# Performance work log

Hardware: AMD Instinct MI355X
Metric: run time of the kernel (lower is better)

The kernel has to match this reference:

```python
import jax, jax.numpy as jnp
import numpy as np
from jax import lax

N_GRAPHS = 256
N_NODES = 128      # nodes per graph (fixed-size batching)
N_TPLT = 16
N_TPLT_NODES = 10
N_FEAT = 128
AVG_DEG = 8
EPS = 0.1          # entropic regularization for the GW solver
OUTER_ITERS = 5    # outer mirror-descent (entropic GW) iterations
SINKHORN_ITERS = 20


def setup_inputs() -> dict:
    key = jax.random.key(0)
    k1, k2, k3, k4, k5 = jax.random.split(key, 5)
    x = jax.random.normal(k1, (N_GRAPHS * N_NODES, N_FEAT), jnp.float32)
    # per-graph random edges with global node ids (PyG convention)
    n_e = N_NODES * AVG_DEG
    src = jax.random.randint(k2, (N_GRAPHS, n_e), 0, N_NODES)
    dst = jax.random.randint(k3, (N_GRAPHS, n_e), 0, N_NODES)
    off = (jnp.arange(N_GRAPHS) * N_NODES)[:, None]
    edge_index = jnp.stack([(src + off).reshape(-1), (dst + off).reshape(-1)]).astype(jnp.int32)
    batch = jnp.repeat(jnp.arange(N_GRAPHS, dtype=jnp.int32), N_NODES)
    # template parameters (symmetric uniform adjacencies, normal features, zero q0 -> uniform weights)
    A0 = jax.random.uniform(k4, (N_TPLT, N_TPLT_NODES, N_TPLT_NODES), jnp.float32)
    tplt_adjacencies = 0.5 * (A0 + jnp.swapaxes(A0, 1, 2))
    tplt_features = jax.random.normal(k5, (N_TPLT, N_TPLT_NODES, N_FEAT), jnp.float32)
    q0 = jnp.zeros((N_TPLT, N_TPLT_NODES), jnp.float32)
    return {"x": x, "edge_index": edge_index, "batch": batch,
            "tplt_adjacencies": tplt_adjacencies, "tplt_features": tplt_features, "q0": q0}


def _gw_distances(C1, C2, p, q):
    # C1: [B,N,N] graph adjacencies, C2: [T,M,M] templates, p: [N], q: [T,M]
    # square-loss GW decomposition (Peyre et al.): f1=a^2, f2=b^2, h1=a, h2=2b
    B, N = C1.shape[0], C1.shape[1]
    T, M = C2.shape[0], C2.shape[1]
    f1p = jnp.einsum('bij,j->bi', C1 * C1, p)          # [B,N]
    f2q = jnp.einsum('tij,tj->ti', C2 * C2, q)         # [T,M]
    constC = f1p[:, None, :, None] + f2q[None, :, None, :]  # [B,T,N,M]

    def tens(P):
        # constC - h1(C1) P h2(C2)^T
        cross = jnp.einsum('bik,btkm,tjm->btij', C1, P, 2.0 * C2)
        return constC - cross

    P0 = jnp.broadcast_to(p[None, None, :, None] * q[None, :, None, :], (B, T, N, M))

    def outer(P, _):
        cost = 2.0 * tens(P)                     # GW gradient
        K = jnp.exp(-cost / EPS)                 # [B,T,N,M]
        u0 = jnp.ones((B, T, N), K.dtype)
        v0 = jnp.ones((B, T, M), K.dtype)

        def inner(carry, _):
            u, v = carry
            u = p[None, None, :] / jnp.einsum('btnm,btm->btn', K, v)
            v = q[None, :, :] / jnp.einsum('btnm,btn->btm', K, u)
            return (u, v), None

        (u, v), _ = lax.scan(inner, (u0, v0), None, length=SINKHORN_ITERS)
        P = u[..., :, None] * K * v[..., None, :]
        return P, None

    P, _ = lax.scan(outer, P0, None, length=OUTER_ITERS)
    return jnp.sum(tens(P) * P, axis=(2, 3))     # [B,T]


def reference(x, edge_index, batch, tplt_adjacencies, tplt_features, q0):
    # q = softmax(q0, dim=1): template node weights
    q = jax.nn.softmax(q0, axis=1)
    # dense per-graph adjacency from the sparse edge list
    g = batch[edge_index[0]]
    src = edge_index[0] - g * N_NODES
    dst = edge_index[1] - g * N_NODES
    C1 = jnp.zeros((N_GRAPHS, N_NODES, N_NODES), x.dtype)
    C1 = C1.at[g, src, dst].set(1.0)
    C1 = jnp.maximum(C1, jnp.swapaxes(C1, 1, 2))  # undirected
    p = jnp.full((N_NODES,), 1.0 / N_NODES, x.dtype)  # uniform graph node weights
    # fused=False: pure Gromov-Wasserstein, node features are not used
    return _gw_distances(C1, tplt_adjacencies, p, q)
```

## Files before the change

### kernel.cpp

```cpp
#include <hip/hip_runtime.h>

#define NGRAPH 256
#define NN     128
#define NT     16
#define NM     10
#define OUTER_IT 5
#define SINK_IT  20

#define SC1  28.85390081777927f
#define SC2  57.70780163555854f

typedef unsigned long long u64;
typedef float v2f __attribute__((ext_vector_type(2)));
typedef float v4f __attribute__((ext_vector_type(4)));

static __device__ __forceinline__ v2f pkfma(v2f a, v2f b, v2f c) {
  return __builtin_elementwise_fma(a, b, c);
}
static __device__ __forceinline__ v2f bc2(float s) { return (v2f){s, s}; }

template <int CTRL>
__device__ __forceinline__ float dpp_add(float a) {
  int t = __builtin_amdgcn_update_dpp(0, __float_as_int(a), CTRL, 0xf, 0xf, true);
  return a + __int_as_float(t);
}
__device__ __forceinline__ float allsum32(float x) {
  x = dpp_add<0xB1>(x);
  x = dpp_add<0x4E>(x);
  x = dpp_add<0x141>(x);
  x = dpp_add<0x140>(x);
  int sw = __builtin_amdgcn_ds_swizzle(__float_as_int(x), 0x401F);
  return x + __int_as_float(sw);
}

__global__ __launch_bounds__(64, 2)
void tgw_kernel(const int* __restrict__ ei,
                const float* __restrict__ tadj,
                const float* __restrict__ q0g,
                float* __restrict__ out,
                int E, int ne) {
  const int lane = threadIdx.x;
  const int p    = lane >> 5;
  const int sub  = lane & 31;
  const int b    = blockIdx.x >> 3;
  const int t0   = (blockIdx.x & 7) * 2;

  __shared__ __align__(16) unsigned adj[NN][4];
  __shared__ __align__(16) float Pls[2][NN][12];
  __shared__ __align__(16) v2f C2T[2][NM][6];
  __shared__ float q0s[2][NM];

  for (int i = lane; i < NN * 4; i += 64) (&adj[0][0])[i] = 0u;
  for (int i = lane; i < 2 * NM * 5; i += 64) {
    int tt = i / 50, r = i % 50, m = r / 5, jp = r % 5;
    const float* bp = tadj + (t0 + tt) * NM * NM + m;
    C2T[tt][m][jp] = (v2f){bp[(2 * jp) * NM], bp[(2 * jp + 1) * NM]} * SC2;
  }
  if (lane < 2 * NM) q0s[lane / NM][lane % NM] = q0g[t0 * NM + lane];
  __syncthreads();

  const int* srcp = ei;
  const int* dstp = ei + E;
  const int ebase = b * ne;
  for (int e = lane; e < ne; e += 64) {
    int s = srcp[ebase + e] & (NN - 1);
    int d = dstp[ebase + e] & (NN - 1);
    atomicOr(&adj[s][d >> 5], 1u << (d & 31));
    atomicOr(&adj[d][s >> 5], 1u << (s & 31));
  }
  __syncthreads();

  float qv[NM];
  {
    float mx = q0s[p][0];
    #pragma unroll
    for (int j = 1; j < NM; ++j) mx = fmaxf(mx, q0s[p][j]);
    float s = 0.f;
    #pragma unroll
    for (int j = 0; j < NM; ++j) { qv[j] = __expf(q0s[p][j] - mx); s += qv[j]; }
    float inv = __builtin_amdgcn_rcpf(s);
    #pragma unroll
    for (int j = 0; j < NM; ++j) qv[j] *= inv;
  }
  v2f q2[5];
  #pragma unroll
  for (int jp = 0; jp < 5; ++jp) q2[jp] = (v2f){qv[2 * jp], qv[2 * jp + 1]};

  v2f fq2[5], qC2T[5];
  {
    #pragma unroll
    for (int jp = 0; jp < 5; ++jp) { fq2[jp] = (v2f){0.f, 0.f}; qC2T[jp] = (v2f){0.f, 0.f}; }
    #pragma unroll
    for (int m = 0; m < NM; ++m) {
      v2f qb = bc2(qv[m]);
      #pragma unroll
      for (int jp = 0; jp < 5; ++jp) {
        v2f c = C2T[p][m][jp];
        fq2[jp]  = pkfma(c * c, qb, fq2[jp]);
        qC2T[jp] = pkfma(c, qb, qC2T[jp]);
      }
    }
    const float f = -1.0f / (4.0f * SC1);
    #pragma unroll
    for (int jp = 0; jp < 5; ++jp) fq2[jp] *= f;
  }

  const float pw = 1.0f / 128.0f;
  float f1p[4], m1f1[4];
  #pragma unroll
  for (int c = 0; c < 4; ++c) {
    uint4 mm = *(const uint4*)&adj[sub + 32 * c][0];
    u64 m0 = mm.x | ((u64)mm.y << 32), m1 = mm.z | ((u64)mm.w << 32);
    f1p[c]  = (float)(__popcll(m0) + __popcll(m1)) * pw;
    m1f1[c] = -SC1 * f1p[c];
  }

  const float* Pbase = &Pls[p][0][0];
  auto gatherRow = [&](int r, v2f* S2) {
    uint4 mm = *(const uint4*)&adj[r][0];
    u64 m0 = mm.x | ((u64)mm.y << 32), m1 = mm.z | ((u64)mm.w << 32);
    #pragma unroll
    for (int h = 0; h < 5; ++h) S2[h] = (v2f){0.f, 0.f};
    while (m0) {
      int k = (int)__builtin_ctzll(m0); m0 &= m0 - 1;
      const float* row = Pbase + k * 12;
      v4f A = *(const v4f*)row;
      v4f B = *(const v4f*)(row + 4);
      v2f C = *(const v2f*)(row + 8);
      S2[0] += A.xy; S2[1] += A.zw; S2[2] += B.xy; S2[3] += B.zw; S2[4] += C;
    }
    while (m1) {
      int k = 64 + (int)__builtin_ctzll(m1); m1 &= m1 - 1;
      const float* row = Pbase + k * 12;
      v4f A = *(const v4f*)row;
      v4f B = *(const v4f*)(row + 4);
      v2f C = *(const v2f*)(row + 8);
      S2[0] += A.xy; S2[1] += A.zw; S2[2] += B.xy; S2[3] += B.zw; S2[4] += C;
    }
  };

  auto costFromS = [&](float Sm[4][NM], v2f arg2[4][5]) {
    #pragma unroll
    for (int c = 0; c < 4; ++c) {
      v2f ib = fq2[0] + bc2(m1f1[c]);
      arg2[c][0] = ib;
      #pragma unroll
      for (int jp = 1; jp < 5; ++jp) arg2[c][jp] = fq2[jp] + bc2(m1f1[c]);
    }
    #pragma unroll
    for (int m = 0; m < NM; ++m) {
      v4f X = *(const v4f*)&C2T[p][m][0];
      v4f Y = *(const v4f*)&C2T[p][m][2];
      v2f Z = *(const v2f*)&C2T[p][m][4];
      #pragma unroll
      for (int c = 0; c < 4; ++c) {
        v2f sb = bc2(Sm[c][m]);
        arg2[c][0] = pkfma(sb, X.xy, arg2[c][0]);
        arg2[c][1] = pkfma(sb, X.zw, arg2[c][1]);
        arg2[c][2] = pkfma(sb, Y.xy, arg2[c][2]);
        arg2[c][3] = pkfma(sb, Y.zw, arg2[c][3]);
        arg2[c][4] = pkfma(sb, Z,    arg2[c][4]);
      }
    }
  };

  v2f K2[4][5], v2[5], arg2[4][5];
  float uu[4];

  for (int o = 0; o < OUTER_IT; ++o) {
    if (o == 0) {
      #pragma unroll
      for (int c = 0; c < 4; ++c) {
        v2f fb = bc2(f1p[c]);
        v2f ob = bc2(m1f1[c]);
        #pragma unroll
        for (int jp = 0; jp < 5; ++jp)
          arg2[c][jp] = pkfma(fb, qC2T[jp], fq2[jp] + ob);
      }
    } else {
      float Sm[4][NM];
      #pragma unroll
      for (int c = 0; c < 4; ++c) {
        v2f S2[5];
        gatherRow(sub + 32 * c, S2);
        #pragma unroll
        for (int h = 0; h < 5; ++h) { Sm[c][2 * h] = S2[h].x; Sm[c][2 * h + 1] = S2[h].y; }
      }
      costFromS(Sm, arg2);
    }
    #pragma unroll
    for (int c = 0; c < 4; ++c)
      #pragma unroll
      for (int jp = 0; jp < 5; ++jp)
        K2[c][jp] = (v2f){exp2f(arg2[c][jp].x), exp2f(arg2[c][jp].y)};

    #pragma unroll
    for (int jp = 0; jp < 5; ++jp) v2[jp] = (v2f){1.f, 1.f};
    for (int it = 0; it < SINK_IT; ++it) {
      #pragma unroll
      for (int c = 0; c < 4; ++c) {
        v2f d2 = K2[c][0] * v2[0];
        d2 = pkfma(K2[c][1], v2[1], d2);
        d2 = pkfma(K2[c][2], v2[2], d2);
        d2 = pkfma(K2[c][3], v2[3], d2);
        d2 = pkfma(K2[c][4], v2[4], d2);
        uu[c] = pw * __builtin_amdgcn_rcpf(d2.x + d2.y);
      }
      #pragma unroll
      for (int jp = 0; jp < 5; ++jp) {
        v2f w2 = K2[0][jp] * bc2(uu[0]);
        w2 = pkfma(K2[1][jp], bc2(uu[1]), w2);
        w2 = pkfma(K2[2][jp], bc2(uu[2]), w2);
        w2 = pkfma(K2[3][jp], bc2(uu[3]), w2);
        float cx = allsum32(w2.x);
        float cy = allsum32(w2.y);
        v2[jp] = (v2f){q2[jp].x * __builtin_amdgcn_rcpf(cx),
                       q2[jp].y * __builtin_amdgcn_rcpf(cy)};
      }
    }

    __syncthreads();
    #pragma unroll
    for (int c = 0; c < 4; ++c) {
      v2f ub = bc2(uu[c]);
      v2f x0 = K2[c][0] * ub * v2[0];
      v2f x1 = K2[c][1] * ub * v2[1];
      v2f x2 = K2[c][2] * ub * v2[2];
      v2f x3 = K2[c][3] * ub * v2[3];
      v2f x4 = K2[c][4] * ub * v2[4];
      float* row = &Pls[p][sub + 32 * c][0];
      *(v4f*)row       = (v4f){x0.x, x0.y, x1.x, x1.y};
      *(v4f*)(row + 4) = (v4f){x2.x, x2.y, x3.x, x3.y};
      *(v2f*)(row + 8) = x4;
    }
    __syncthreads();
  }

  float acc = 0.f;
  {
    float Sm[4][NM];
    #pragma unroll
    for (int c = 0; c < 4; ++c) {
      v2f S2[5];
      gatherRow(sub + 32 * c, S2);
      #pragma unroll
      for (int h = 0; h < 5; ++h) { Sm[c][2 * h] = S2[h].x; Sm[c][2 * h + 1] = S2[h].y; }
    }
    costFromS(Sm, arg2);
    const v2f nf = bc2(-1.0f / SC1);
    v2f acc2 = (v2f){0.f, 0.f};
    #pragma unroll
    for (int c = 0; c < 4; ++c) {
      v2f ub = bc2(uu[c]);
      #pragma unroll
      for (int jp = 0; jp < 5; ++jp) {
        v2f Pv = K2[c][jp] * ub * v2[jp];
        acc2 = pkfma(arg2[c][jp] * nf, Pv, acc2);
      }
    }
    acc = acc2.x + acc2.y;
  }
  float total = allsum32(acc);
  if (sub == 0) out[b * NT + t0 + p] = total;
}

extern "C" void kernel_launch(void* const* d_in, const int* in_sizes, int n_in,
                              void* d_out, int out_size, void* d_ws, size_t ws_size,
                              hipStream_t stream) {
  const int* ei   = (const int*)d_in[1];
  const float* c2 = (const float*)d_in[3];
  const float* q0 = (const float*)d_in[5];
  float* out      = (float*)d_out;
  const int E  = in_sizes[1] / 2;
  const int ne = E / NGRAPH;
  tgw_kernel<<<dim3(NGRAPH * 8), dim3(64), 0, stream>>>(ei, c2, q0, out, E, ne);
}
```

Before: 199.9 us.

## Interleave four row gathers, pad P stride, use permlane16 swap reduction

```diff
diff --git a/kernel.cpp b/kernel.cpp
--- a/kernel.cpp
+++ b/kernel.cpp
@@ -10,6 +10,8 @@
 #define SC1  28.85390081777927f
 #define SC2  57.70780163555854f
 
+#define PSTR 14
+
 typedef unsigned long long u64;
 typedef float v2f __attribute__((ext_vector_type(2)));
 typedef float v4f __attribute__((ext_vector_type(4)));
@@ -24,13 +26,34 @@
   int t = __builtin_amdgcn_update_dpp(0, __float_as_int(a), CTRL, 0xf, 0xf, true);
   return a + __int_as_float(t);
 }
+
+#if defined(__has_builtin)
+#if __has_builtin(__builtin_amdgcn_permlane16_swap)
+#define HAVE_PL16SWAP 1
+#endif
+#endif
+__device__ __forceinline__ float xor16_add(float x) {
+#ifdef HAVE_PL16SWAP
+  auto rr = __builtin_amdgcn_permlane16_swap(__float_as_int(x), __float_as_int(x),
+                                             false, false);
+  return __int_as_float((int)rr[0]) + __int_as_float((int)rr[1]);
+#else
+  float a = x, b = x, r;
+  asm("s_nop 1\n\t"
+      "v_permlane16_swap_b32 %1, %2\n\t"
+      "s_nop 1\n\t"
+      "v_add_f32 %0, %1, %2"
+      : "=v"(r), "+v"(a), "+v"(b));
+  return r;
+#endif
+}
+
 __device__ __forceinline__ float allsum32(float x) {
   x = dpp_add<0xB1>(x);
   x = dpp_add<0x4E>(x);
   x = dpp_add<0x141>(x);
   x = dpp_add<0x140>(x);
-  int sw = __builtin_amdgcn_ds_swizzle(__float_as_int(x), 0x401F);
-  return x + __int_as_float(sw);
+  return xor16_add(x);
 }
 
 __global__ __launch_bounds__(64, 2)
@@ -46,7 +69,7 @@
   const int t0   = (blockIdx.x & 7) * 2;
 
   __shared__ __align__(16) unsigned adj[NN][4];
-  __shared__ __align__(16) float Pls[2][NN][12];
+  __shared__ __align__(16) float Pls[2][NN][PSTR];
   __shared__ __align__(16) v2f C2T[2][NM][6];
   __shared__ float q0s[2][NM];
 
@@ -82,9 +105,10 @@
     #pragma unroll
     for (int j = 0; j < NM; ++j) qv[j] *= inv;
   }
-  v2f q2[5];
+  v2f q2d[5];
   #pragma unroll
-  for (int jp = 0; jp < 5; ++jp) q2[jp] = (v2f){qv[2 * jp], qv[2 * jp + 1]};
+  for (int jp = 0; jp < 5; ++jp)
+    q2d[jp] = (v2f){qv[2 * jp] * 128.f, qv[2 * jp + 1] * 128.f};
 
   v2f fq2[5], qC2T[5];
   {
@@ -116,36 +140,63 @@
   }
 
   const float* Pbase = &Pls[p][0][0];
-  auto gatherRow = [&](int r, v2f* S2) {
-    uint4 mm = *(const uint4*)&adj[r][0];
-    u64 m0 = mm.x | ((u64)mm.y << 32), m1 = mm.z | ((u64)mm.w << 32);
-    #pragma unroll
-    for (int h = 0; h < 5; ++h) S2[h] = (v2f){0.f, 0.f};
-    while (m0) {
-      int k = (int)__builtin_ctzll(m0); m0 &= m0 - 1;
-      const float* row = Pbase + k * 12;
-      v4f A = *(const v4f*)row;
-      v4f B = *(const v4f*)(row + 4);
-      v2f C = *(const v2f*)(row + 8);
-      S2[0] += A.xy; S2[1] += A.zw; S2[2] += B.xy; S2[3] += B.zw; S2[4] += C;
-    }
-    while (m1) {
-      int k = 64 + (int)__builtin_ctzll(m1); m1 &= m1 - 1;
-      const float* row = Pbase + k * 12;
-      v4f A = *(const v4f*)row;
-      v4f B = *(const v4f*)(row + 4);
-      v2f C = *(const v2f*)(row + 8);
-      S2[0] += A.xy; S2[1] += A.zw; S2[2] += B.xy; S2[3] += B.zw; S2[4] += C;
+
+  auto gather4 = [&](float Sm[4][NM]) {
+    v2f S2[4][5];
+    u64 M0[4], M1[4];
+    #pragma unroll
+    for (int c = 0; c < 4; ++c) {
+      uint4 mm = *(const uint4*)&adj[sub + 32 * c][0];
+      M0[c] = mm.x | ((u64)mm.y << 32);
+      M1[c] = mm.z | ((u64)mm.w << 32);
+      #pragma unroll
+      for (int h = 0; h < 5; ++h) S2[c][h] = (v2f){0.f, 0.f};
+    }
+    while (M0[0] && M0[1] && M0[2] && M0[3]) {
+      #pragma unroll
+      for (int c = 0; c < 4; ++c) {
+        int k = (int)__builtin_ctzll(M0[c]); M0[c] &= M0[c] - 1;
+        const float* row = Pbase + k * PSTR;
+        #pragma unroll
+        for (int h = 0; h < 5; ++h) S2[c][h] += *(const v2f*)(row + 2 * h);
+      }
+    }
+    #pragma unroll
+    for (int c = 0; c < 4; ++c) {
+      while (M0[c]) {
+        int k = (int)__builtin_ctzll(M0[c]); M0[c] &= M0[c] - 1;
+        const float* row = Pbase + k * PSTR;
+        #pragma unroll
+        for (int h = 0; h < 5; ++h) S2[c][h] += *(const v2f*)(row + 2 * h);
+      }
+    }
+    while (M1[0] && M1[1] && M1[2] && M1[3]) {
+      #pragma unroll
+      for (int c = 0; c < 4; ++c) {
+        int k = 64 + (int)__builtin_ctzll(M1[c]); M1[c] &= M1[c] - 1;
+        const float* row = Pbase + k * PSTR;
+        #pragma unroll
+        for (int h = 0; h < 5; ++h) S2[c][h] += *(const v2f*)(row + 2 * h);
+      }
+    }
+    #pragma unroll
+    for (int c = 0; c < 4; ++c) {
+      while (M1[c]) {
+        int k = 64 + (int)__builtin_ctzll(M1[c]); M1[c] &= M1[c] - 1;
+        const float* row = Pbase + k * PSTR;
+        #pragma unroll
+        for (int h = 0; h < 5; ++h) S2[c][h] += *(const v2f*)(row + 2 * h);
+      }
+      #pragma unroll
+      for (int h = 0; h < 5; ++h) { Sm[c][2 * h] = S2[c][h].x; Sm[c][2 * h + 1] = S2[c][h].y; }
     }
   };
 
   auto costFromS = [&](float Sm[4][NM], v2f arg2[4][5]) {
     #pragma unroll
     for (int c = 0; c < 4; ++c) {
-      v2f ib = fq2[0] + bc2(m1f1[c]);
-      arg2[c][0] = ib;
-      #pragma unroll
-      for (int jp = 1; jp < 5; ++jp) arg2[c][jp] = fq2[jp] + bc2(m1f1[c]);
+      #pragma unroll
+      for (int jp = 0; jp < 5; ++jp) arg2[c][jp] = fq2[jp] + bc2(m1f1[c]);
     }
     #pragma unroll
     for (int m = 0; m < NM; ++m) {
@@ -179,13 +230,7 @@
       }
     } else {
       float Sm[4][NM];
-      #pragma unroll
-      for (int c = 0; c < 4; ++c) {
-        v2f S2[5];
-        gatherRow(sub + 32 * c, S2);
-        #pragma unroll
-        for (int h = 0; h < 5; ++h) { Sm[c][2 * h] = S2[h].x; Sm[c][2 * h + 1] = S2[h].y; }
-      }
+      gather4(Sm);
       costFromS(Sm, arg2);
     }
     #pragma unroll
@@ -204,7 +249,7 @@
         d2 = pkfma(K2[c][2], v2[2], d2);
         d2 = pkfma(K2[c][3], v2[3], d2);
         d2 = pkfma(K2[c][4], v2[4], d2);
-        uu[c] = pw * __builtin_amdgcn_rcpf(d2.x + d2.y);
+        uu[c] = __builtin_amdgcn_rcpf(d2.x + d2.y);
       }
       #pragma unroll
       for (int jp = 0; jp < 5; ++jp) {
@@ -214,23 +259,25 @@
         w2 = pkfma(K2[3][jp], bc2(uu[3]), w2);
         float cx = allsum32(w2.x);
         float cy = allsum32(w2.y);
-        v2[jp] = (v2f){q2[jp].x * __builtin_amdgcn_rcpf(cx),
-                       q2[jp].y * __builtin_amdgcn_rcpf(cy)};
+        v2[jp] = (v2f){q2d[jp].x * __builtin_amdgcn_rcpf(cx),
+                       q2d[jp].y * __builtin_amdgcn_rcpf(cy)};
       }
     }
 
     __syncthreads();
     #pragma unroll
     for (int c = 0; c < 4; ++c) {
-      v2f ub = bc2(uu[c]);
+      v2f ub = bc2(uu[c] * pw);
       v2f x0 = K2[c][0] * ub * v2[0];
       v2f x1 = K2[c][1] * ub * v2[1];
       v2f x2 = K2[c][2] * ub * v2[2];
       v2f x3 = K2[c][3] * ub * v2[3];
       v2f x4 = K2[c][4] * ub * v2[4];
       float* row = &Pls[p][sub + 32 * c][0];
-      *(v4f*)row       = (v4f){x0.x, x0.y, x1.x, x1.y};
-      *(v4f*)(row + 4) = (v4f){x2.x, x2.y, x3.x, x3.y};
+      *(v2f*)(row + 0) = x0;
+      *(v2f*)(row + 2) = x1;
+      *(v2f*)(row + 4) = x2;
+      *(v2f*)(row + 6) = x3;
       *(v2f*)(row + 8) = x4;
     }
     __syncthreads();
@@ -239,19 +286,13 @@
   float acc = 0.f;
   {
     float Sm[4][NM];
-    #pragma unroll
-    for (int c = 0; c < 4; ++c) {
-      v2f S2[5];
-      gatherRow(sub + 32 * c, S2);
-      #pragma unroll
-      for (int h = 0; h < 5; ++h) { Sm[c][2 * h] = S2[h].x; Sm[c][2 * h + 1] = S2[h].y; }
-    }
+    gather4(Sm);
     costFromS(Sm, arg2);
     const v2f nf = bc2(-1.0f / SC1);
     v2f acc2 = (v2f){0.f, 0.f};
     #pragma unroll
     for (int c = 0; c < 4; ++c) {
-      v2f ub = bc2(uu[c]);
+      v2f ub = bc2(uu[c] * pw);
       #pragma unroll
       for (int jp = 0; jp < 5; ++jp) {
         v2f Pv = K2[c][jp] * ub * v2[jp];
```

Result: slower. 232.7 us (+16.4%).

## Map one (graph, template) pair per wavefront with 64-lane permlane reductions

Applied to the files above, without the earlier changes.

```diff
diff --git a/kernel.cpp b/kernel.cpp
--- a/kernel.cpp
+++ b/kernel.cpp
@@ -10,6 +10,8 @@
 #define SC1  28.85390081777927f
 #define SC2  57.70780163555854f
 
+#define PSTR 12
+
 typedef unsigned long long u64;
 typedef float v2f __attribute__((ext_vector_type(2)));
 typedef float v4f __attribute__((ext_vector_type(4)));
@@ -24,39 +26,77 @@
   int t = __builtin_amdgcn_update_dpp(0, __float_as_int(a), CTRL, 0xf, 0xf, true);
   return a + __int_as_float(t);
 }
-__device__ __forceinline__ float allsum32(float x) {
+
+#if defined(__has_builtin)
+#if __has_builtin(__builtin_amdgcn_permlane16_swap)
+#define HAVE_PL16SWAP 1
+#endif
+#if __has_builtin(__builtin_amdgcn_permlane32_swap)
+#define HAVE_PL32SWAP 1
+#endif
+#endif
+__device__ __forceinline__ float xor16_add(float x) {
+#ifdef HAVE_PL16SWAP
+  auto rr = __builtin_amdgcn_permlane16_swap(__float_as_int(x), __float_as_int(x),
+                                             false, false);
+  return __int_as_float((int)rr[0]) + __int_as_float((int)rr[1]);
+#else
+  float a = x, b = x, r;
+  asm("s_nop 1\n\t"
+      "v_permlane16_swap_b32 %1, %2\n\t"
+      "s_nop 1\n\t"
+      "v_add_f32 %0, %1, %2"
+      : "=v"(r), "+v"(a), "+v"(b));
+  return r;
+#endif
+}
+__device__ __forceinline__ float xor32_add(float x) {
+#ifdef HAVE_PL32SWAP
+  auto rr = __builtin_amdgcn_permlane32_swap(__float_as_int(x), __float_as_int(x),
+                                             false, false);
+  return __int_as_float((int)rr[0]) + __int_as_float((int)rr[1]);
+#else
+  float a = x, b = x, r;
+  asm("s_nop 1\n\t"
+      "v_permlane32_swap_b32 %1, %2\n\t"
+      "s_nop 1\n\t"
+      "v_add_f32 %0, %1, %2"
+      : "=v"(r), "+v"(a), "+v"(b));
+  return r;
+#endif
+}
+
+__device__ __forceinline__ float allsum64(float x) {
   x = dpp_add<0xB1>(x);
   x = dpp_add<0x4E>(x);
   x = dpp_add<0x141>(x);
   x = dpp_add<0x140>(x);
-  int sw = __builtin_amdgcn_ds_swizzle(__float_as_int(x), 0x401F);
-  return x + __int_as_float(sw);
-}
-
-__global__ __launch_bounds__(64, 2)
+  x = xor16_add(x);
+  return xor32_add(x);
+}
+
+__global__ __launch_bounds__(64, 4)
 void tgw_kernel(const int* __restrict__ ei,
                 const float* __restrict__ tadj,
                 const float* __restrict__ q0g,
                 float* __restrict__ out,
                 int E, int ne) {
   const int lane = threadIdx.x;
-  const int p    = lane >> 5;
-  const int sub  = lane & 31;
-  const int b    = blockIdx.x >> 3;
-  const int t0   = (blockIdx.x & 7) * 2;
+  const int b    = blockIdx.x >> 4;
+  const int t    = blockIdx.x & 15;
 
   __shared__ __align__(16) unsigned adj[NN][4];
-  __shared__ __align__(16) float Pls[2][NN][12];
-  __shared__ __align__(16) v2f C2T[2][NM][6];
-  __shared__ float q0s[2][NM];
+  __shared__ __align__(16) float Pls[NN][PSTR];
+  __shared__ __align__(16) v2f C2T[NM][6];
+  __shared__ float q0s[NM];
 
   for (int i = lane; i < NN * 4; i += 64) (&adj[0][0])[i] = 0u;
-  for (int i = lane; i < 2 * NM * 5; i += 64) {
-    int tt = i / 50, r = i % 50, m = r / 5, jp = r % 5;
-    const float* bp = tadj + (t0 + tt) * NM * NM + m;
-    C2T[tt][m][jp] = (v2f){bp[(2 * jp) * NM], bp[(2 * jp + 1) * NM]} * SC2;
-  }
-  if (lane < 2 * NM) q0s[lane / NM][lane % NM] = q0g[t0 * NM + lane];
+  if (lane < NM * 5) {
+    int m = lane / 5, jp = lane % 5;
+    const float* bp = tadj + t * NM * NM + m;
+    C2T[m][jp] = (v2f){bp[(2 * jp) * NM], bp[(2 * jp + 1) * NM]} * SC2;
+  }
+  if (lane < NM) q0s[lane] = q0g[t * NM + lane];
   __syncthreads();
 
   const int* srcp = ei;
@@ -72,19 +112,20 @@
 
   float qv[NM];
   {
-    float mx = q0s[p][0];
-    #pragma unroll
-    for (int j = 1; j < NM; ++j) mx = fmaxf(mx, q0s[p][j]);
+    float mx = q0s[0];
+    #pragma unroll
+    for (int j = 1; j < NM; ++j) mx = fmaxf(mx, q0s[j]);
     float s = 0.f;
     #pragma unroll
-    for (int j = 0; j < NM; ++j) { qv[j] = __expf(q0s[p][j] - mx); s += qv[j]; }
+    for (int j = 0; j < NM; ++j) { qv[j] = __expf(q0s[j] - mx); s += qv[j]; }
     float inv = __builtin_amdgcn_rcpf(s);
     #pragma unroll
     for (int j = 0; j < NM; ++j) qv[j] *= inv;
   }
-  v2f q2[5];
+  v2f q2d[5];
   #pragma unroll
-  for (int jp = 0; jp < 5; ++jp) q2[jp] = (v2f){qv[2 * jp], qv[2 * jp + 1]};
+  for (int jp = 0; jp < 5; ++jp)
+    q2d[jp] = (v2f){qv[2 * jp] * 128.f, qv[2 * jp + 1] * 128.f};
 
   v2f fq2[5], qC2T[5];
   {
@@ -95,7 +136,7 @@
       v2f qb = bc2(qv[m]);
       #pragma unroll
       for (int jp = 0; jp < 5; ++jp) {
-        v2f c = C2T[p][m][jp];
+        v2f c = C2T[m][jp];
         fq2[jp]  = pkfma(c * c, qb, fq2[jp]);
         qC2T[jp] = pkfma(c, qb, qC2T[jp]);
       }
@@ -106,16 +147,16 @@
   }
 
   const float pw = 1.0f / 128.0f;
-  float f1p[4], m1f1[4];
+  float f1p[2], m1f1[2];
   #pragma unroll
-  for (int c = 0; c < 4; ++c) {
-    uint4 mm = *(const uint4*)&adj[sub + 32 * c][0];
+  for (int c = 0; c < 2; ++c) {
+    uint4 mm = *(const uint4*)&adj[lane + 64 * c][0];
     u64 m0 = mm.x | ((u64)mm.y << 32), m1 = mm.z | ((u64)mm.w << 32);
     f1p[c]  = (float)(__popcll(m0) + __popcll(m1)) * pw;
     m1f1[c] = -SC1 * f1p[c];
   }
 
-  const float* Pbase = &Pls[p][0][0];
+  const float* Pbase = &Pls[0][0];
   auto gatherRow = [&](int r, v2f* S2) {
     uint4 mm = *(const uint4*)&adj[r][0];
     u64 m0 = mm.x | ((u64)mm.y << 32), m1 = mm.z | ((u64)mm.w << 32);
@@ -123,7 +164,7 @@
     for (int h = 0; h < 5; ++h) S2[h] = (v2f){0.f, 0.f};
     while (m0) {
       int k = (int)__builtin_ctzll(m0); m0 &= m0 - 1;
-      const float* row = Pbase + k * 12;
+      const float* row = Pbase + k * PSTR;
       v4f A = *(const v4f*)row;
       v4f B = *(const v4f*)(row + 4);
       v2f C = *(const v2f*)(row + 8);
@@ -131,7 +172,7 @@
     }
     while (m1) {
       int k = 64 + (int)__builtin_ctzll(m1); m1 &= m1 - 1;
-      const float* row = Pbase + k * 12;
+      const float* row = Pbase + k * PSTR;
       v4f A = *(const v4f*)row;
       v4f B = *(const v4f*)(row + 4);
       v2f C = *(const v2f*)(row + 8);
@@ -139,21 +180,19 @@
     }
   };
 
-  auto costFromS = [&](float Sm[4][NM], v2f arg2[4][5]) {
-    #pragma unroll
-    for (int c = 0; c < 4; ++c) {
-      v2f ib = fq2[0] + bc2(m1f1[c]);
-      arg2[c][0] = ib;
-      #pragma unroll
-      for (int jp = 1; jp < 5; ++jp) arg2[c][jp] = fq2[jp] + bc2(m1f1[c]);
+  auto costFromS = [&](float Sm[2][NM], v2f arg2[2][5]) {
+    #pragma unroll
+    for (int c = 0; c < 2; ++c) {
+      #pragma unroll
+      for (int jp = 0; jp < 5; ++jp) arg2[c][jp] = fq2[jp] + bc2(m1f1[c]);
     }
     #pragma unroll
     for (int m = 0; m < NM; ++m) {
-      v4f X = *(const v4f*)&C2T[p][m][0];
-      v4f Y = *(const v4f*)&C2T[p][m][2];
-      v2f Z = *(const v2f*)&C2T[p][m][4];
-      #pragma unroll
-      for (int c = 0; c < 4; ++c) {
+      v4f X = *(const v4f*)&C2T[m][0];
+      v4f Y = *(const v4f*)&C2T[m][2];
+      v2f Z = *(const v2f*)&C2T[m][4];
+      #pragma unroll
+      for (int c = 0; c < 2; ++c) {
         v2f sb = bc2(Sm[c][m]);
         arg2[c][0] = pkfma(sb, X.xy, arg2[c][0]);
         arg2[c][1] = pkfma(sb, X.zw, arg2[c][1]);
@@ -164,13 +203,13 @@
     }
   };
 
-  v2f K2[4][5], v2[5], arg2[4][5];
-  float uu[4];
+  v2f K2[2][5], v2[5], arg2[2][5];
+  float uu[2];
 
   for (int o = 0; o < OUTER_IT; ++o) {
     if (o == 0) {
       #pragma unroll
-      for (int c = 0; c < 4; ++c) {
+      for (int c = 0; c < 2; ++c) {
         v2f fb = bc2(f1p[c]);
         v2f ob = bc2(m1f1[c]);
         #pragma unroll
@@ -178,18 +217,18 @@
           arg2[c][jp] = pkfma(fb, qC2T[jp], fq2[jp] + ob);
       }
     } else {
-      float Sm[4][NM];
-      #pragma unroll
-      for (int c = 0; c < 4; ++c) {
+      float Sm[2][NM];
+      #pragma unroll
+      for (int c = 0; c < 2; ++c) {
         v2f S2[5];
-        gatherRow(sub + 32 * c, S2);
+        gatherRow(lane + 64 * c, S2);
         #pragma unroll
         for (int h = 0; h < 5; ++h) { Sm[c][2 * h] = S2[h].x; Sm[c][2 * h + 1] = S2[h].y; }
       }
       costFromS(Sm, arg2);
     }
     #pragma unroll
-    for (int c = 0; c < 4; ++c)
+    for (int c = 0; c < 2; ++c)
       #pragma unroll
       for (int jp = 0; jp < 5; ++jp)
         K2[c][jp] = (v2f){exp2f(arg2[c][jp].x), exp2f(arg2[c][jp].y)};
@@ -198,37 +237,35 @@
     for (int jp = 0; jp < 5; ++jp) v2[jp] = (v2f){1.f, 1.f};
     for (int it = 0; it < SINK_IT; ++it) {
       #pragma unroll
-      for (int c = 0; c < 4; ++c) {
+      for (int c = 0; c < 2; ++c) {
         v2f d2 = K2[c][0] * v2[0];
         d2 = pkfma(K2[c][1], v2[1], d2);
         d2 = pkfma(K2[c][2], v2[2], d2);
         d2 = pkfma(K2[c][3], v2[3], d2);
         d2 = pkfma(K2[c][4], v2[4], d2);
-        uu[c] = pw * __builtin_amdgcn_rcpf(d2.x + d2.y);
+        uu[c] = __builtin_amdgcn_rcpf(d2.x + d2.y);
       }
       #pragma unroll
       for (int jp = 0; jp < 5; ++jp) {
         v2f w2 = K2[0][jp] * bc2(uu[0]);
         w2 = pkfma(K2[1][jp], bc2(uu[1]), w2);
-        w2 = pkfma(K2[2][jp], bc2(uu[2]), w2);
-        w2 = pkfma(K2[3][jp], bc2(uu[3]), w2);
-        float cx = allsum32(w2.x);
-        float cy = allsum32(w2.y);
-        v2[jp] = (v2f){q2[jp].x * __builtin_amdgcn_rcpf(cx),
-                       q2[jp].y * __builtin_amdgcn_rcpf(cy)};
+        float cx = allsum64(w2.x);
+        float cy = allsum64(w2.y);
+        v2[jp] = (v2f){q2d[jp].x * __builtin_amdgcn_rcpf(cx),
+                       q2d[jp].y * __builtin_amdgcn_rcpf(cy)};
       }
     }
 
     __syncthreads();
     #pragma unroll
-    for (int c = 0; c < 4; ++c) {
-      v2f ub = bc2(uu[c]);
+    for (int c = 0; c < 2; ++c) {
+      v2f ub = bc2(uu[c] * pw);
       v2f x0 = K2[c][0] * ub * v2[0];
       v2f x1 = K2[c][1] * ub * v2[1];
       v2f x2 = K2[c][2] * ub * v2[2];
       v2f x3 = K2[c][3] * ub * v2[3];
       v2f x4 = K2[c][4] * ub * v2[4];
-      float* row = &Pls[p][sub + 32 * c][0];
+      float* row = &Pls[lane + 64 * c][0];
       *(v4f*)row       = (v4f){x0.x, x0.y, x1.x, x1.y};
       *(v4f*)(row + 4) = (v4f){x2.x, x2.y, x3.x, x3.y};
       *(v2f*)(row + 8) = x4;
@@ -238,11 +275,11 @@
 
   float acc = 0.f;
   {
-    float Sm[4][NM];
-    #pragma unroll
-    for (int c = 0; c < 4; ++c) {
+    float Sm[2][NM];
+    #pragma unroll
+    for (int c = 0; c < 2; ++c) {
       v2f S2[5];
-      gatherRow(sub + 32 * c, S2);
+      gatherRow(lane + 64 * c, S2);
       #pragma unroll
       for (int h = 0; h < 5; ++h) { Sm[c][2 * h] = S2[h].x; Sm[c][2 * h + 1] = S2[h].y; }
     }
@@ -250,8 +287,8 @@
     const v2f nf = bc2(-1.0f / SC1);
     v2f acc2 = (v2f){0.f, 0.f};
     #pragma unroll
-    for (int c = 0; c < 4; ++c) {
-      v2f ub = bc2(uu[c]);
+    for (int c = 0; c < 2; ++c) {
+      v2f ub = bc2(uu[c] * pw);
       #pragma unroll
       for (int jp = 0; jp < 5; ++jp) {
         v2f Pv = K2[c][jp] * ub * v2[jp];
@@ -260,8 +297,8 @@
     }
     acc = acc2.x + acc2.y;
   }
-  float total = allsum32(acc);
-  if (sub == 0) out[b * NT + t0 + p] = total;
+  float total = allsum64(acc);
+  if (lane == 0) out[b * NT + t] = total;
 }
 
 extern "C" void kernel_launch(void* const* d_in, const int* in_sizes, int n_in,
@@ -273,5 +310,5 @@
   float* out      = (float*)d_out;
   const int E  = in_sizes[1] / 2;
   const int ne = E / NGRAPH;
-  tgw_kernel<<<dim3(NGRAPH * 8), dim3(64), 0, stream>>>(ei, c2, q0, out, E, ne);
-}
+  tgw_kernel<<<dim3(NGRAPH * NT), dim3(64), 0, stream>>>(ei, c2, q0, out, E, ne);
+}
```

Measured after the change: 251.6 us. 1.26x slower.

## Map four templates per block with 16 lanes each and 8 rows per lane

Applied to the files above, without the earlier changes.

```diff
diff --git a/kernel.cpp b/kernel.cpp
--- a/kernel.cpp
+++ b/kernel.cpp
@@ -10,6 +10,8 @@
 #define SC1  28.85390081777927f
 #define SC2  57.70780163555854f
 
+#define PSTR 12
+
 typedef unsigned long long u64;
 typedef float v2f __attribute__((ext_vector_type(2)));
 typedef float v4f __attribute__((ext_vector_type(4)));
@@ -24,39 +26,38 @@
   int t = __builtin_amdgcn_update_dpp(0, __float_as_int(a), CTRL, 0xf, 0xf, true);
   return a + __int_as_float(t);
 }
-__device__ __forceinline__ float allsum32(float x) {
+__device__ __forceinline__ float allsum16(float x) {
   x = dpp_add<0xB1>(x);
   x = dpp_add<0x4E>(x);
   x = dpp_add<0x141>(x);
   x = dpp_add<0x140>(x);
-  int sw = __builtin_amdgcn_ds_swizzle(__float_as_int(x), 0x401F);
-  return x + __int_as_float(sw);
-}
-
-__global__ __launch_bounds__(64, 2)
+  return x;
+}
+
+__global__ __launch_bounds__(64, 1)
 void tgw_kernel(const int* __restrict__ ei,
                 const float* __restrict__ tadj,
                 const float* __restrict__ q0g,
                 float* __restrict__ out,
                 int E, int ne) {
   const int lane = threadIdx.x;
-  const int p    = lane >> 5;
-  const int sub  = lane & 31;
-  const int b    = blockIdx.x >> 3;
-  const int t0   = (blockIdx.x & 7) * 2;
+  const int g    = lane >> 4;
+  const int sub  = lane & 15;
+  const int b    = blockIdx.x >> 2;
+  const int t0   = (blockIdx.x & 3) * 4;
 
   __shared__ __align__(16) unsigned adj[NN][4];
-  __shared__ __align__(16) float Pls[2][NN][12];
-  __shared__ __align__(16) v2f C2T[2][NM][6];
-  __shared__ float q0s[2][NM];
+  __shared__ __align__(16) float Pls[4][NN][PSTR];
+  __shared__ __align__(16) v2f C2T[4][NM][6];
+  __shared__ float q0s[4][NM];
 
   for (int i = lane; i < NN * 4; i += 64) (&adj[0][0])[i] = 0u;
-  for (int i = lane; i < 2 * NM * 5; i += 64) {
+  for (int i = lane; i < 4 * NM * 5; i += 64) {
     int tt = i / 50, r = i % 50, m = r / 5, jp = r % 5;
     const float* bp = tadj + (t0 + tt) * NM * NM + m;
     C2T[tt][m][jp] = (v2f){bp[(2 * jp) * NM], bp[(2 * jp + 1) * NM]} * SC2;
   }
-  if (lane < 2 * NM) q0s[lane / NM][lane % NM] = q0g[t0 * NM + lane];
+  if (lane < 4 * NM) q0s[lane / NM][lane % NM] = q0g[t0 * NM + lane];
   __syncthreads();
 
   const int* srcp = ei;
@@ -72,19 +73,20 @@
 
   float qv[NM];
   {
-    float mx = q0s[p][0];
-    #pragma unroll
-    for (int j = 1; j < NM; ++j) mx = fmaxf(mx, q0s[p][j]);
+    float mx = q0s[g][0];
+    #pragma unroll
+    for (int j = 1; j < NM; ++j) mx = fmaxf(mx, q0s[g][j]);
     float s = 0.f;
     #pragma unroll
-    for (int j = 0; j < NM; ++j) { qv[j] = __expf(q0s[p][j] - mx); s += qv[j]; }
+    for (int j = 0; j < NM; ++j) { qv[j] = __expf(q0s[g][j] - mx); s += qv[j]; }
     float inv = __builtin_amdgcn_rcpf(s);
     #pragma unroll
     for (int j = 0; j < NM; ++j) qv[j] *= inv;
   }
-  v2f q2[5];
+  v2f q2d[5];
   #pragma unroll
-  for (int jp = 0; jp < 5; ++jp) q2[jp] = (v2f){qv[2 * jp], qv[2 * jp + 1]};
+  for (int jp = 0; jp < 5; ++jp)
+    q2d[jp] = (v2f){qv[2 * jp] * 128.f, qv[2 * jp + 1] * 128.f};
 
   v2f fq2[5], qC2T[5];
   {
@@ -95,7 +97,7 @@
       v2f qb = bc2(qv[m]);
       #pragma unroll
       for (int jp = 0; jp < 5; ++jp) {
-        v2f c = C2T[p][m][jp];
+        v2f c = C2T[g][m][jp];
         fq2[jp]  = pkfma(c * c, qb, fq2[jp]);
         qC2T[jp] = pkfma(c, qb, qC2T[jp]);
       }
@@ -106,16 +108,16 @@
   }
 
   const float pw = 1.0f / 128.0f;
-  float f1p[4], m1f1[4];
+  float f1p[8], m1f1[8];
   #pragma unroll
-  for (int c = 0; c < 4; ++c) {
-    uint4 mm = *(const uint4*)&adj[sub + 32 * c][0];
+  for (int c = 0; c < 8; ++c) {
+    uint4 mm = *(const uint4*)&adj[sub + 16 * c][0];
     u64 m0 = mm.x | ((u64)mm.y << 32), m1 = mm.z | ((u64)mm.w << 32);
     f1p[c]  = (float)(__popcll(m0) + __popcll(m1)) * pw;
     m1f1[c] = -SC1 * f1p[c];
   }
 
-  const float* Pbase = &Pls[p][0][0];
+  const float* Pbase = &Pls[g][0][0];
   auto gatherRow = [&](int r, v2f* S2) {
     uint4 mm = *(const uint4*)&adj[r][0];
     u64 m0 = mm.x | ((u64)mm.y << 32), m1 = mm.z | ((u64)mm.w << 32);
@@ -123,7 +125,7 @@
     for (int h = 0; h < 5; ++h) S2[h] = (v2f){0.f, 0.f};
     while (m0) {
       int k = (int)__builtin_ctzll(m0); m0 &= m0 - 1;
-      const float* row = Pbase + k * 12;
+      const float* row = Pbase + k * PSTR;
       v4f A = *(const v4f*)row;
       v4f B = *(const v4f*)(row + 4);
       v2f C = *(const v2f*)(row + 8);
@@ -131,7 +133,7 @@
     }
     while (m1) {
       int k = 64 + (int)__builtin_ctzll(m1); m1 &= m1 - 1;
-      const float* row = Pbase + k * 12;
+      const float* row = Pbase + k * PSTR;
       v4f A = *(const v4f*)row;
       v4f B = *(const v4f*)(row + 4);
       v2f C = *(const v2f*)(row + 8);
@@ -139,96 +141,90 @@
     }
   };
 
-  auto costFromS = [&](float Sm[4][NM], v2f arg2[4][5]) {
-    #pragma unroll
-    for (int c = 0; c < 4; ++c) {
-      v2f ib = fq2[0] + bc2(m1f1[c]);
-      arg2[c][0] = ib;
-      #pragma unroll
-      for (int jp = 1; jp < 5; ++jp) arg2[c][jp] = fq2[jp] + bc2(m1f1[c]);
-    }
+  auto costRow = [&](const v2f* S2, float m1f1c, v2f* a) {
+    #pragma unroll
+    for (int jp = 0; jp < 5; ++jp) a[jp] = fq2[jp] + bc2(m1f1c);
     #pragma unroll
     for (int m = 0; m < NM; ++m) {
-      v4f X = *(const v4f*)&C2T[p][m][0];
-      v4f Y = *(const v4f*)&C2T[p][m][2];
-      v2f Z = *(const v2f*)&C2T[p][m][4];
-      #pragma unroll
-      for (int c = 0; c < 4; ++c) {
-        v2f sb = bc2(Sm[c][m]);
-        arg2[c][0] = pkfma(sb, X.xy, arg2[c][0]);
-        arg2[c][1] = pkfma(sb, X.zw, arg2[c][1]);
-        arg2[c][2] = pkfma(sb, Y.xy, arg2[c][2]);
-        arg2[c][3] = pkfma(sb, Y.zw, arg2[c][3]);
-        arg2[c][4] = pkfma(sb, Z,    arg2[c][4]);
-      }
+      v4f X = *(const v4f*)&C2T[g][m][0];
+      v4f Y = *(const v4f*)&C2T[g][m][2];
+      v2f Z = *(const v2f*)&C2T[g][m][4];
+      float sm = (m & 1) ? S2[m >> 1].y : S2[m >> 1].x;
+      v2f sb = bc2(sm);
+      a[0] = pkfma(sb, X.xy, a[0]);
+      a[1] = pkfma(sb, X.zw, a[1]);
+      a[2] = pkfma(sb, Y.xy, a[2]);
+      a[3] = pkfma(sb, Y.zw, a[3]);
+      a[4] = pkfma(sb, Z,    a[4]);
     }
   };
 
-  v2f K2[4][5], v2[5], arg2[4][5];
-  float uu[4];
+  v2f K2[8][5], v2[5];
+  float uu[8];
 
   for (int o = 0; o < OUTER_IT; ++o) {
     if (o == 0) {
       #pragma unroll
-      for (int c = 0; c < 4; ++c) {
+      for (int c = 0; c < 8; ++c) {
         v2f fb = bc2(f1p[c]);
         v2f ob = bc2(m1f1[c]);
         #pragma unroll
-        for (int jp = 0; jp < 5; ++jp)
-          arg2[c][jp] = pkfma(fb, qC2T[jp], fq2[jp] + ob);
+        for (int jp = 0; jp < 5; ++jp) {
+          v2f a = pkfma(fb, qC2T[jp], fq2[jp] + ob);
+          K2[c][jp] = (v2f){exp2f(a.x), exp2f(a.y)};
+        }
       }
     } else {
-      float Sm[4][NM];
-      #pragma unroll
-      for (int c = 0; c < 4; ++c) {
-        v2f S2[5];
-        gatherRow(sub + 32 * c, S2);
+      #pragma unroll
+      for (int cp = 0; cp < 4; ++cp) {
+        const int c0 = 2 * cp, c1 = c0 + 1;
+        v2f S0[5], S1[5], a0[5], a1[5];
+        gatherRow(sub + 16 * c0, S0);
+        gatherRow(sub + 16 * c1, S1);
+        costRow(S0, m1f1[c0], a0);
+        costRow(S1, m1f1[c1], a1);
         #pragma unroll
-        for (int h = 0; h < 5; ++h) { Sm[c][2 * h] = S2[h].x; Sm[c][2 * h + 1] = S2[h].y; }
-      }
-      costFromS(Sm, arg2);
-    }
-    #pragma unroll
-    for (int c = 0; c < 4; ++c)
-      #pragma unroll
-      for (int jp = 0; jp < 5; ++jp)
-        K2[c][jp] = (v2f){exp2f(arg2[c][jp].x), exp2f(arg2[c][jp].y)};
+        for (int jp = 0; jp < 5; ++jp) {
+          K2[c0][jp] = (v2f){exp2f(a0[jp].x), exp2f(a0[jp].y)};
+          K2[c1][jp] = (v2f){exp2f(a1[jp].x), exp2f(a1[jp].y)};
+        }
+      }
+    }
 
     #pragma unroll
     for (int jp = 0; jp < 5; ++jp) v2[jp] = (v2f){1.f, 1.f};
     for (int it = 0; it < SINK_IT; ++it) {
       #pragma unroll
-      for (int c = 0; c < 4; ++c) {
+      for (int c = 0; c < 8; ++c) {
         v2f d2 = K2[c][0] * v2[0];
         d2 = pkfma(K2[c][1], v2[1], d2);
         d2 = pkfma(K2[c][2], v2[2], d2);
         d2 = pkfma(K2[c][3], v2[3], d2);
         d2 = pkfma(K2[c][4], v2[4], d2);
-        uu[c] = pw * __builtin_amdgcn_rcpf(d2.x + d2.y);
+        uu[c] = __builtin_amdgcn_rcpf(d2.x + d2.y);
       }
       #pragma unroll
       for (int jp = 0; jp < 5; ++jp) {
         v2f w2 = K2[0][jp] * bc2(uu[0]);
-        w2 = pkfma(K2[1][jp], bc2(uu[1]), w2);
-        w2 = pkfma(K2[2][jp], bc2(uu[2]), w2);
-        w2 = pkfma(K2[3][jp], bc2(uu[3]), w2);
-        float cx = allsum32(w2.x);
-        float cy = allsum32(w2.y);
-        v2[jp] = (v2f){q2[jp].x * __builtin_amdgcn_rcpf(cx),
-                       q2[jp].y * __builtin_amdgcn_rcpf(cy)};
+        #pragma unroll
+        for (int c = 1; c < 8; ++c) w2 = pkfma(K2[c][jp], bc2(uu[c]), w2);
+        float cx = allsum16(w2.x);
+        float cy = allsum16(w2.y);
+        v2[jp] = (v2f){q2d[jp].x * __builtin_amdgcn_rcpf(cx),
+                       q2d[jp].y * __builtin_amdgcn_rcpf(cy)};
       }
     }
 
     __syncthreads();
     #pragma unroll
-    for (int c = 0; c < 4; ++c) {
-      v2f ub = bc2(uu[c]);
+    for (int c = 0; c < 8; ++c) {
+      v2f ub = bc2(uu[c] * pw);
       v2f x0 = K2[c][0] * ub * v2[0];
       v2f x1 = K2[c][1] * ub * v2[1];
       v2f x2 = K2[c][2] * ub * v2[2];
       v2f x3 = K2[c][3] * ub * v2[3];
       v2f x4 = K2[c][4] * ub * v2[4];
-      float* row = &Pls[p][sub + 32 * c][0];
+      float* row = &Pls[g][sub + 16 * c][0];
       *(v4f*)row       = (v4f){x0.x, x0.y, x1.x, x1.y};
       *(v4f*)(row + 4) = (v4f){x2.x, x2.y, x3.x, x3.y};
       *(v2f*)(row + 8) = x4;
@@ -236,32 +232,28 @@
     __syncthreads();
   }
 
-  float acc = 0.f;
+  v2f acc2 = (v2f){0.f, 0.f};
   {
-    float Sm[4][NM];
-    #pragma unroll
-    for (int c = 0; c < 4; ++c) {
-      v2f S2[5];
-      gatherRow(sub + 32 * c, S2);
-      #pragma unroll
-      for (int h = 0; h < 5; ++h) { Sm[c][2 * h] = S2[h].x; Sm[c][2 * h + 1] = S2[h].y; }
-    }
-    costFromS(Sm, arg2);
     const v2f nf = bc2(-1.0f / SC1);
-    v2f acc2 = (v2f){0.f, 0.f};
-    #pragma unroll
-    for (int c = 0; c < 4; ++c) {
-      v2f ub = bc2(uu[c]);
+    #pragma unroll
+    for (int cp = 0; cp < 4; ++cp) {
+      const int c0 = 2 * cp, c1 = c0 + 1;
+      v2f S0[5], S1[5], a0[5], a1[5];
+      gatherRow(sub + 16 * c0, S0);
+      gatherRow(sub + 16 * c1, S1);
+      costRow(S0, m1f1[c0], a0);
+      costRow(S1, m1f1[c1], a1);
+      v2f ub0 = bc2(uu[c0] * pw);
+      v2f ub1 = bc2(uu[c1] * pw);
       #pragma unroll
       for (int jp = 0; jp < 5; ++jp) {
-        v2f Pv = K2[c][jp] * ub * v2[jp];
-        acc2 = pkfma(arg2[c][jp] * nf, Pv, acc2);
-      }
-    }
-    acc = acc2.x + acc2.y;
-  }
-  float total = allsum32(acc);
-  if (sub == 0) out[b * NT + t0 + p] = total;
+        acc2 = pkfma(a0[jp] * nf, K2[c0][jp] * ub0 * v2[jp], acc2);
+        acc2 = pkfma(a1[jp] * nf, K2[c1][jp] * ub1 * v2[jp], acc2);
+      }
+    }
+  }
+  float total = allsum16(acc2.x + acc2.y);
+  if (sub == 0) out[b * NT + t0 + g] = total;
 }
 
 extern "C" void kernel_launch(void* const* d_in, const int* in_sizes, int n_in,
@@ -273,5 +265,5 @@
   float* out      = (float*)d_out;
   const int E  = in_sizes[1] / 2;
   const int ne = E / NGRAPH;
-  tgw_kernel<<<dim3(NGRAPH * 8), dim3(64), 0, stream>>>(ei, c2, q0, out, E, ne);
-}
+  tgw_kernel<<<dim3(NGRAPH * 4), dim3(64), 0, stream>>>(ei, c2, q0, out, E, ne);
+}
```

New measurement: 208.5 us. 4.3% more time.
